# Kernel optimization log

Hardware: AMD Instinct MI355X
Metric: run time of the kernel (lower is better)

The kernel has to match this reference:

```python
import jax, jax.numpy as jnp
import numpy as np

# HGIN_classifier: two relational-GIN layers with ReLU between.
# FastRGIN layer math (relational GIN, eps=0, single-linear MLP):
#   agg_r[i] = sum_{(j->i) with edge_type r} x[j]          (per-relation neighbor sum)
#   out[i]   = (1+eps) * x[i] @ W_self + sum_r agg_r[i] @ W_r + b

N = 100000      # nodes
E = 1600000     # edges (avg degree 16)
R = 2           # relations (follower / following)
DIN, DH, DOUT = 128, 256, 2
EPS = 0.0


def setup_inputs() -> dict:
    key = jax.random.key(0)
    ks = jax.random.split(key, 8)
    x = jax.random.normal(ks[0], (N, DIN), dtype=jnp.float32)
    edge_index = jax.random.randint(ks[1], (2, E), 0, N, dtype=jnp.int64)
    edge_type = jax.random.randint(ks[2], (E,), 0, R, dtype=jnp.int64)
    s1 = 1.0 / np.sqrt(DIN).astype(np.float32)
    s2 = 1.0 / np.sqrt(DH).astype(np.float32)
    w1_self = jax.random.normal(ks[3], (DIN, DH), jnp.float32) * s1
    w1_rel = jax.random.normal(ks[4], (R, DIN, DH), jnp.float32) * s1
    b1 = jnp.zeros((DH,), jnp.float32)
    w2_self = jax.random.normal(ks[5], (DH, DOUT), jnp.float32) * s2
    w2_rel = jax.random.normal(ks[6], (R, DH, DOUT), jnp.float32) * s2
    b2 = jnp.zeros((DOUT,), jnp.float32)
    return {"x": x, "edge_index": edge_index, "edge_type": edge_type,
            "w1_self": w1_self, "w1_rel": w1_rel, "b1": b1,
            "w2_self": w2_self, "w2_rel": w2_rel, "b2": b2}


def _rgin_layer(x, src, dst, etype, w_self, w_rel, b):
    n = x.shape[0]
    r = w_rel.shape[0]
    # fused (node, relation) segment id so one segment_sum handles all relations
    seg = dst * r + etype                                   # [E]
    agg = jax.ops.segment_sum(x[src], seg, num_segments=n * r)  # [N*R, d_in]
    agg = agg.reshape(n, r, -1)                              # [N, R, d_in]
    return (1.0 + EPS) * (x @ w_self) + jnp.einsum('nri,rio->no', agg, w_rel) + b


def reference(x, edge_index, edge_type, w1_self, w1_rel, b1, w2_self, w2_rel, b2):
    src, dst = edge_index[0], edge_index[1]
    h = jax.nn.relu(_rgin_layer(x, src, dst, edge_type, w1_self, w1_rel, b1))
    out = _rgin_layer(h, src, dst, edge_type, w2_self, w2_rel, b2)
    return out
```

## Files before the change

kernel.cpp:

```cpp
#include <hip/hip_runtime.h>


typedef _Float16 f16;
typedef _Float16 f16x2 __attribute__((ext_vector_type(2)));
typedef _Float16 f16x4 __attribute__((ext_vector_type(4)));
typedef _Float16 f16x8 __attribute__((ext_vector_type(8)));
typedef float    f32x4 __attribute__((ext_vector_type(4)));

constexpr int NN   = 100000;
constexpr int NR   = NN * 2;
constexpr int NB   = 512;
constexpr int BSH  = 9;
constexpr int CHUNK = 8192;

__global__ void zero_small(int* __restrict__ gcnt) {
  int t = threadIdx.x;
  if (t < NB) gcnt[t] = 0;
}

__global__ void bucketA(const int* __restrict__ dst, const int* __restrict__ et,
                        int* __restrict__ gcnt, int E) {
  __shared__ int h[NB];
  int t = threadIdx.x;
  for (int b = t; b < NB; b += 256) h[b] = 0;
  __syncthreads();
  int lo = blockIdx.x * CHUNK, hi = min(E, lo + CHUNK);
  for (int e = lo + t; e < hi; e += 256)
    atomicAdd(&h[(dst[e] * 2 + et[e]) >> BSH], 1);
  __syncthreads();
  for (int b = t; b < NB; b += 256) {
    int c = h[b];
    if (c) atomicAdd(&gcnt[b], c);
  }
}

__global__ void bscan(const int* __restrict__ gcnt, int* __restrict__ bstart,
                      int* __restrict__ gbase) {
  __shared__ int s[NB];
  int t = threadIdx.x;
  int v = gcnt[t];
  s[t] = v;
  __syncthreads();
  #pragma unroll
  for (int o = 1; o < NB; o <<= 1) {
    int u = (t >= o) ? s[t - o] : 0;
    __syncthreads();
    s[t] += u;
    __syncthreads();
  }
  bstart[t] = s[t] - v;
  gbase[t]  = s[t] - v;
  if (t == NB - 1) bstart[NB] = s[t];
}

__global__ void bucketB(const int* __restrict__ src, const int* __restrict__ dst,
                        const int* __restrict__ et, int* __restrict__ gbase,
                        int2* __restrict__ ebuf, int E) {
  __shared__ int h[NB], base[NB];
  int t = threadIdx.x;
  for (int b = t; b < NB; b += 256) h[b] = 0;
  __syncthreads();
  int lo = blockIdx.x * CHUNK, hi = min(E, lo + CHUNK);
  for (int e = lo + t; e < hi; e += 256)
    atomicAdd(&h[(dst[e] * 2 + et[e]) >> BSH], 1);
  __syncthreads();
  for (int b = t; b < NB; b += 256) {
    int c = h[b];
    base[b] = c ? atomicAdd(&gbase[b], c) : 0;
    h[b] = 0;
  }
  __syncthreads();
  for (int e = lo + t; e < hi; e += 256) {
    int seg = dst[e] * 2 + et[e];
    int b = seg >> BSH;
    int r = atomicAdd(&h[b], 1);
    ebuf[base[b] + r] = make_int2(src[e], seg);
  }
}

__global__ void bucketC(const int2* __restrict__ ebuf, const int* __restrict__ bstart,
                        int* __restrict__ off, int* __restrict__ srcs) {
  __shared__ int sh[NB], soff[NB], cnt[NB], tmp[256];
  int b = blockIdx.x, t = threadIdx.x;
  int lo = bstart[b], hi = bstart[b + 1];
  for (int s0 = t; s0 < NB; s0 += 256) { sh[s0] = 0; cnt[s0] = 0; }
  __syncthreads();
  for (int e = lo + t; e < hi; e += 256)
    atomicAdd(&sh[ebuf[e].y - (b << BSH)], 1);
  __syncthreads();
  int a0 = sh[2 * t], a1 = sh[2 * t + 1];
  tmp[t] = a0 + a1;
  __syncthreads();
  #pragma unroll
  for (int o = 1; o < 256; o <<= 1) {
    int u = (t >= o) ? tmp[t - o] : 0;
    __syncthreads();
    tmp[t] += u;
    __syncthreads();
  }
  int ex = tmp[t] - (a0 + a1);
  soff[2 * t] = ex;
  soff[2 * t + 1] = ex + a0;
  __syncthreads();
  int g0 = (b << BSH) + 2 * t;
  if (g0 <= NR)     off[g0]     = lo + soff[2 * t];
  if (g0 + 1 <= NR) off[g0 + 1] = lo + soff[2 * t + 1];
  for (int e = lo + t; e < hi; e += 256) {
    int2 p = ebuf[e];
    int s = p.y - (b << BSH);
    int r = atomicAdd(&cnt[s], 1);
    srcs[lo + soff[s] + r] = p.x;
  }
}

__global__ void cvt_x(const float4* __restrict__ xf, f16* __restrict__ xh, int n4) {
  int i = blockIdx.x * blockDim.x + threadIdx.x;
  if (i >= n4) return;
  float4 v = xf[i];
  f16x4 h;
  h.x = (f16)v.x; h.y = (f16)v.y; h.z = (f16)v.z; h.w = (f16)v.w;
  *(f16x4*)(xh + (size_t)i * 4) = h;
}

__global__ void cvt_w(const float* __restrict__ w1s, const float* __restrict__ w1r,
                      f16* __restrict__ w1t) {
  int id = blockIdx.x * blockDim.x + threadIdx.x;
  if (id >= 12 * 256 * 32) return;
  int ks = id >> 13, rem = id & 8191;
  int n = rem >> 5, ki = rem & 31;
  int k = ks * 32 + ki;
  float v = (k < 128) ? w1s[k * 256 + n] : w1r[(k - 128) * 256 + n];
  w1t[id] = (f16)v;
}

__global__ void aggregate(const f16* __restrict__ xh, const int* __restrict__ off,
                          const int* __restrict__ srcs, f16* __restrict__ aggh) {
  int w = (blockIdx.x * blockDim.x + threadIdx.x) >> 6;
  if (w >= NN) return;
  int lane = threadIdx.x & 63;
  int e0 = off[2 * w];
  int e1 = off[2 * w + 1];
  int e2 = off[2 * w + 2];
  float a0 = 0.f, a1 = 0.f, c0 = 0.f, c1 = 0.f;
  int e = e0;
  for (; e + 3 < e1; e += 4) {
    f16x2 v0 = *(const f16x2*)(xh + (long)srcs[e] * 128 + lane * 2);
    f16x2 v1 = *(const f16x2*)(xh + (long)srcs[e + 1] * 128 + lane * 2);
    f16x2 v2 = *(const f16x2*)(xh + (long)srcs[e + 2] * 128 + lane * 2);
    f16x2 v3 = *(const f16x2*)(xh + (long)srcs[e + 3] * 128 + lane * 2);
    a0 += (float)v0.x + (float)v1.x + (float)v2.x + (float)v3.x;
    a1 += (float)v0.y + (float)v1.y + (float)v2.y + (float)v3.y;
  }
  for (; e < e1; ++e) {
    f16x2 v = *(const f16x2*)(xh + (long)srcs[e] * 128 + lane * 2);
    a0 += (float)v.x; a1 += (float)v.y;
  }
  e = e1;
  for (; e + 3 < e2; e += 4) {
    f16x2 v0 = *(const f16x2*)(xh + (long)srcs[e] * 128 + lane * 2);
    f16x2 v1 = *(const f16x2*)(xh + (long)srcs[e + 1] * 128 + lane * 2);
    f16x2 v2 = *(const f16x2*)(xh + (long)srcs[e + 2] * 128 + lane * 2);
    f16x2 v3 = *(const f16x2*)(xh + (long)srcs[e + 3] * 128 + lane * 2);
    c0 += (float)v0.x + (float)v1.x + (float)v2.x + (float)v3.x;
    c1 += (float)v0.y + (float)v1.y + (float)v2.y + (float)v3.y;
  }
  for (; e < e2; ++e) {
    f16x2 v = *(const f16x2*)(xh + (long)srcs[e] * 128 + lane * 2);
    c0 += (float)v.x; c1 += (float)v.y;
  }
  f16* row = aggh + (long)w * 256;
  f16x2 o0; o0.x = (f16)a0; o0.y = (f16)a1;
  f16x2 o1; o1.x = (f16)c0; o1.y = (f16)c1;
  *(f16x2*)(row + lane * 2) = o0;
  *(f16x2*)(row + 128 + lane * 2) = o1;
}

__global__ __launch_bounds__(256) void gemm_mfma(
    const f16* __restrict__ xh, const f16* __restrict__ aggh,
    const f16* __restrict__ w1t,
    const float* __restrict__ b1, const float* __restrict__ w2s,
    const float* __restrict__ w2r, const float* __restrict__ b2,
    float* __restrict__ z2, float* __restrict__ out) {
  __shared__ float zbuf[4][64][6];
  const int t = threadIdx.x;
  const int lane = t & 63, wv = t >> 6;
  const int ml = lane & 15, quad = lane >> 4;
  const long rowBase = (long)blockIdx.x * 64;

  long rowc[4];
  #pragma unroll
  for (int mt = 0; mt < 4; ++mt) {
    long r = rowBase + mt * 16 + ml;
    rowc[mt] = r < NN ? r : (NN - 1);
  }
  const f16* bbase = w1t + (long)(wv * 64 + ml) * 32 + quad * 8;

  f32x4 acc[4][4];
  #pragma unroll
  for (int mt = 0; mt < 4; ++mt)
    #pragma unroll
    for (int nt = 0; nt < 4; ++nt) acc[mt][nt] = (f32x4)(0.f);

  #pragma unroll
  for (int ks = 0; ks < 12; ++ks) {
    f16x8 af[4], bf[4];
    #pragma unroll
    for (int mt = 0; mt < 4; ++mt) {
      const f16* ap = (ks < 4)
          ? (xh + rowc[mt] * 128 + ks * 32 + quad * 8)
          : (aggh + rowc[mt] * 256 + (ks - 4) * 32 + quad * 8);
      af[mt] = *(const f16x8*)ap;
    }
    #pragma unroll
    for (int nt = 0; nt < 4; ++nt)
      bf[nt] = *(const f16x8*)(bbase + (long)ks * 8192 + nt * 16 * 32);
    #pragma unroll
    for (int mt = 0; mt < 4; ++mt)
      #pragma unroll
      for (int nt = 0; nt < 4; ++nt)
        acc[mt][nt] = __builtin_amdgcn_mfma_f32_16x16x32_f16(af[mt], bf[nt],
                                                             acc[mt][nt], 0, 0, 0);
  }

  #pragma unroll
  for (int mt = 0; mt < 4; ++mt) {
    float z[4][6];
    #pragma unroll
    for (int rr = 0; rr < 4; ++rr)
      #pragma unroll
      for (int p = 0; p < 6; ++p) z[rr][p] = 0.f;
    #pragma unroll
    for (int nt = 0; nt < 4; ++nt) {
      int col = wv * 64 + nt * 16 + ml;
      float bb = b1[col];
      float wA = w2r[col * 2 + 0];
      float wB = w2r[col * 2 + 1];
      float wC = w2r[512 + col * 2 + 0];
      float wD = w2r[512 + col * 2 + 1];
      float wE = w2s[col * 2 + 0];
      float wF = w2s[col * 2 + 1];
      #pragma unroll
      for (int rr = 0; rr < 4; ++rr) {
        float h = acc[mt][nt][rr] + bb;
        h = h > 0.f ? h : 0.f;
        z[rr][0] = fmaf(h, wA, z[rr][0]);
        z[rr][1] = fmaf(h, wB, z[rr][1]);
        z[rr][2] = fmaf(h, wC, z[rr][2]);
        z[rr][3] = fmaf(h, wD, z[rr][3]);
        z[rr][4] = fmaf(h, wE, z[rr][4]);
        z[rr][5] = fmaf(h, wF, z[rr][5]);
      }
    }
    #pragma unroll
    for (int rr = 0; rr < 4; ++rr)
      #pragma unroll
      for (int p = 0; p < 6; ++p) {
        float v = z[rr][p];
        v += __shfl_xor(v, 1);
        v += __shfl_xor(v, 2);
        v += __shfl_xor(v, 4);
        v += __shfl_xor(v, 8);
        if (ml == 0) zbuf[wv][mt * 16 + quad * 4 + rr][p] = v;
      }
  }
  __syncthreads();
  for (int i = t; i < 384; i += 256) {
    int r = i / 6, p = i % 6;
    long grow = rowBase + r;
    if (grow < NN) {
      float v = zbuf[0][r][p] + zbuf[1][r][p] + zbuf[2][r][p] + zbuf[3][r][p];
      if (p < 4) z2[grow * 4 + p] = v;
      else       out[grow * 2 + (p - 4)] = v + b2[p - 4];
    }
  }
}

__global__ void gather2(const float* __restrict__ z2, const int* __restrict__ off,
                        const int* __restrict__ srcs, float* __restrict__ out) {
  int tid = blockIdx.x * blockDim.x + threadIdx.x;
  int n = tid >> 2;
  if (n >= NN) return;
  int sub = tid & 3;
  int e0 = off[2 * n];
  int e1 = off[2 * n + 1];
  int e2 = off[2 * n + 2];
  float o0 = 0.f, o1 = 0.f;
  for (int e = e0 + sub; e < e1; e += 4) {
    float2 v = *(const float2*)(z2 + (long)srcs[e] * 4);
    o0 += v.x; o1 += v.y;
  }
  for (int e = e1 + sub; e < e2; e += 4) {
    float2 v = *(const float2*)(z2 + (long)srcs[e] * 4 + 2);
    o0 += v.x; o1 += v.y;
  }
  o0 += __shfl_xor(o0, 1); o1 += __shfl_xor(o1, 1);
  o0 += __shfl_xor(o0, 2); o1 += __shfl_xor(o1, 2);
  if (sub == 0) {
    out[n * 2 + 0] += o0;
    out[n * 2 + 1] += o1;
  }
}

extern "C" void kernel_launch(void* const* d_in, const int* in_sizes, int n_in,
                              void* d_out, int out_size, void* d_ws, size_t ws_size,
                              hipStream_t stream) {
  const float* x   = (const float*)d_in[0];
  const int*   ei  = (const int*)d_in[1];
  const int*   et  = (const int*)d_in[2];
  const float* w1s = (const float*)d_in[3];
  const float* w1r = (const float*)d_in[4];
  const float* b1  = (const float*)d_in[5];
  const float* w2s = (const float*)d_in[6];
  const float* w2r = (const float*)d_in[7];
  const float* b2  = (const float*)d_in[8];
  float* out = (float*)d_out;
  const int E = in_sizes[2];
  const int* src = ei;
  const int* dst = ei + E;

  f16*   aggh = (f16*)d_ws;
  f16*   xh   = aggh + (size_t)NN * 256;
  f16*   w1t  = xh + (size_t)NN * 128;
  float* z2   = (float*)(w1t + 12 * 256 * 32);
  int2*  ebuf = (int2*)(z2 + (size_t)NN * 4);
  int*   srcs = (int*)(ebuf + E);
  int*   off  = srcs + E;
  int*   gcnt = off + NR + 1;
  int*   bstart = gcnt + NB;
  int*   gbase  = bstart + NB + 1;

  int nblk = (E + CHUNK - 1) / CHUNK;
  zero_small<<<1, 512, 0, stream>>>(gcnt);
  bucketA<<<nblk, 256, 0, stream>>>(dst, et, gcnt, E);
  bscan<<<1, 512, 0, stream>>>(gcnt, bstart, gbase);
  bucketB<<<nblk, 256, 0, stream>>>(src, dst, et, gbase, ebuf, E);
  bucketC<<<NB, 256, 0, stream>>>(ebuf, bstart, off, srcs);

  int n4 = NN * 128 / 4;
  cvt_x<<<(n4 + 255) / 256, 256, 0, stream>>>((const float4*)x, xh, n4);
  cvt_w<<<(12 * 256 * 32 + 255) / 256, 256, 0, stream>>>(w1s, w1r, w1t);

  aggregate<<<(NN * 64 + 255) / 256, 256, 0, stream>>>(xh, off, srcs, aggh);

  gemm_mfma<<<(NN + 63) / 64, 256, 0, stream>>>(xh, aggh, w1t, b1, w2s, w2r, b2,
                                                z2, out);

  gather2<<<(NN * 4 + 255) / 256, 256, 0, stream>>>(z2, off, srcs, out);
}
```

Before: 385.9 us.

## Pack bucket entries, merge convert kernels, widen gathers, stage GEMM tiles in LDS

Bucket entries are packed into one int (src shifted left plus the local segment), which halves the ebuf traffic. The two conversion kernels become one launch. The aggregate kernel now has each half-wave load 8-byte f16x4 chunks of different edges and combines the halves with a cross-lane shuffle, so each load instruction fetches two neighbor rows. The layer-1 GEMM stages A and B tiles in padded, double-buffered LDS with register prefetch, replacing the per-wave direct global fragment loads, at the cost of extra barriers and more shared memory per block.

```diff
diff --git a/kernel.cpp b/kernel.cpp
--- a/kernel.cpp
+++ b/kernel.cpp
@@ -12,6 +12,7 @@
 constexpr int NB   = 512;
 constexpr int BSH  = 9;
 constexpr int CHUNK = 8192;
+constexpr int RP   = 40;
 
 __global__ void zero_small(int* __restrict__ gcnt) {
   int t = threadIdx.x;
@@ -55,7 +56,7 @@
 
 __global__ void bucketB(const int* __restrict__ src, const int* __restrict__ dst,
                         const int* __restrict__ et, int* __restrict__ gbase,
-                        int2* __restrict__ ebuf, int E) {
+                        int* __restrict__ ebuf, int E) {
   __shared__ int h[NB], base[NB];
   int t = threadIdx.x;
   for (int b = t; b < NB; b += 256) h[b] = 0;
@@ -74,11 +75,11 @@
     int seg = dst[e] * 2 + et[e];
     int b = seg >> BSH;
     int r = atomicAdd(&h[b], 1);
-    ebuf[base[b] + r] = make_int2(src[e], seg);
-  }
-}
-
-__global__ void bucketC(const int2* __restrict__ ebuf, const int* __restrict__ bstart,
+    ebuf[base[b] + r] = (src[e] << BSH) | (seg & (NB - 1));
+  }
+}
+
+__global__ void bucketC(const int* __restrict__ ebuf, const int* __restrict__ bstart,
                         int* __restrict__ off, int* __restrict__ srcs) {
   __shared__ int sh[NB], soff[NB], cnt[NB], tmp[256];
   int b = blockIdx.x, t = threadIdx.x;
@@ -86,7 +87,7 @@
   for (int s0 = t; s0 < NB; s0 += 256) { sh[s0] = 0; cnt[s0] = 0; }
   __syncthreads();
   for (int e = lo + t; e < hi; e += 256)
-    atomicAdd(&sh[ebuf[e].y - (b << BSH)], 1);
+    atomicAdd(&sh[ebuf[e] & (NB - 1)], 1);
   __syncthreads();
   int a0 = sh[2 * t], a1 = sh[2 * t + 1];
   tmp[t] = a0 + a1;
@@ -106,31 +107,32 @@
   if (g0 <= NR)     off[g0]     = lo + soff[2 * t];
   if (g0 + 1 <= NR) off[g0 + 1] = lo + soff[2 * t + 1];
   for (int e = lo + t; e < hi; e += 256) {
-    int2 p = ebuf[e];
-    int s = p.y - (b << BSH);
+    int p = ebuf[e];
+    int s = p & (NB - 1);
     int r = atomicAdd(&cnt[s], 1);
-    srcs[lo + soff[s] + r] = p.x;
-  }
-}
-
-__global__ void cvt_x(const float4* __restrict__ xf, f16* __restrict__ xh, int n4) {
+    srcs[lo + soff[s] + r] = ((unsigned)p) >> BSH;
+  }
+}
+
+__global__ void cvt_all(const float4* __restrict__ xf, f16* __restrict__ xh,
+                        const float* __restrict__ w1s, const float* __restrict__ w1r,
+                        f16* __restrict__ w1t, int n4) {
   int i = blockIdx.x * blockDim.x + threadIdx.x;
-  if (i >= n4) return;
-  float4 v = xf[i];
-  f16x4 h;
-  h.x = (f16)v.x; h.y = (f16)v.y; h.z = (f16)v.z; h.w = (f16)v.w;
-  *(f16x4*)(xh + (size_t)i * 4) = h;
-}
-
-__global__ void cvt_w(const float* __restrict__ w1s, const float* __restrict__ w1r,
-                      f16* __restrict__ w1t) {
-  int id = blockIdx.x * blockDim.x + threadIdx.x;
-  if (id >= 12 * 256 * 32) return;
-  int ks = id >> 13, rem = id & 8191;
-  int n = rem >> 5, ki = rem & 31;
-  int k = ks * 32 + ki;
-  float v = (k < 128) ? w1s[k * 256 + n] : w1r[(k - 128) * 256 + n];
-  w1t[id] = (f16)v;
+  if (i < n4) {
+    float4 v = xf[i];
+    f16x4 h;
+    h.x = (f16)v.x; h.y = (f16)v.y; h.z = (f16)v.z; h.w = (f16)v.w;
+    *(f16x4*)(xh + (size_t)i * 4) = h;
+  } else {
+    int id = i - n4;
+    if (id < 12 * 256 * 32) {
+      int ks = id >> 13, rem = id & 8191;
+      int n = rem >> 5, ki = rem & 31;
+      int k = ks * 32 + ki;
+      float v = (k < 128) ? w1s[k * 256 + n] : w1r[(k - 128) * 256 + n];
+      w1t[id] = (f16)v;
+    }
+  }
 }
 
 __global__ void aggregate(const f16* __restrict__ xh, const int* __restrict__ off,
@@ -138,41 +140,66 @@
   int w = (blockIdx.x * blockDim.x + threadIdx.x) >> 6;
   if (w >= NN) return;
   int lane = threadIdx.x & 63;
+  int h = lane >> 5, c = lane & 31;
   int e0 = off[2 * w];
   int e1 = off[2 * w + 1];
   int e2 = off[2 * w + 2];
-  float a0 = 0.f, a1 = 0.f, c0 = 0.f, c1 = 0.f;
+  float ax = 0.f, ay = 0.f, az = 0.f, aw = 0.f;
+  float bx = 0.f, by = 0.f, bz = 0.f, bw = 0.f;
+
   int e = e0;
-  for (; e + 3 < e1; e += 4) {
-    f16x2 v0 = *(const f16x2*)(xh + (long)srcs[e] * 128 + lane * 2);
-    f16x2 v1 = *(const f16x2*)(xh + (long)srcs[e + 1] * 128 + lane * 2);
-    f16x2 v2 = *(const f16x2*)(xh + (long)srcs[e + 2] * 128 + lane * 2);
-    f16x2 v3 = *(const f16x2*)(xh + (long)srcs[e + 3] * 128 + lane * 2);
-    a0 += (float)v0.x + (float)v1.x + (float)v2.x + (float)v3.x;
-    a1 += (float)v0.y + (float)v1.y + (float)v2.y + (float)v3.y;
-  }
-  for (; e < e1; ++e) {
-    f16x2 v = *(const f16x2*)(xh + (long)srcs[e] * 128 + lane * 2);
-    a0 += (float)v.x; a1 += (float)v.y;
+  for (; e + 7 < e1; e += 8) {
+    f16x4 v0 = *(const f16x4*)(xh + (long)srcs[e     + h] * 128 + c * 4);
+    f16x4 v1 = *(const f16x4*)(xh + (long)srcs[e + 2 + h] * 128 + c * 4);
+    f16x4 v2 = *(const f16x4*)(xh + (long)srcs[e + 4 + h] * 128 + c * 4);
+    f16x4 v3 = *(const f16x4*)(xh + (long)srcs[e + 6 + h] * 128 + c * 4);
+    ax += (float)v0.x + (float)v1.x + (float)v2.x + (float)v3.x;
+    ay += (float)v0.y + (float)v1.y + (float)v2.y + (float)v3.y;
+    az += (float)v0.z + (float)v1.z + (float)v2.z + (float)v3.z;
+    aw += (float)v0.w + (float)v1.w + (float)v2.w + (float)v3.w;
+  }
+  for (; e + 1 < e1; e += 2) {
+    f16x4 v = *(const f16x4*)(xh + (long)srcs[e + h] * 128 + c * 4);
+    ax += (float)v.x; ay += (float)v.y; az += (float)v.z; aw += (float)v.w;
+  }
+  if (e < e1) {
+    f16x4 v = *(const f16x4*)(xh + (long)srcs[e] * 128 + c * 4);
+    if (h == 0) { ax += (float)v.x; ay += (float)v.y; az += (float)v.z; aw += (float)v.w; }
   }
   e = e1;
-  for (; e + 3 < e2; e += 4) {
-    f16x2 v0 = *(const f16x2*)(xh + (long)srcs[e] * 128 + lane * 2);
-    f16x2 v1 = *(const f16x2*)(xh + (long)srcs[e + 1] * 128 + lane * 2);
-    f16x2 v2 = *(const f16x2*)(xh + (long)srcs[e + 2] * 128 + lane * 2);
-    f16x2 v3 = *(const f16x2*)(xh + (long)srcs[e + 3] * 128 + lane * 2);
-    c0 += (float)v0.x + (float)v1.x + (float)v2.x + (float)v3.x;
-    c1 += (float)v0.y + (float)v1.y + (float)v2.y + (float)v3.y;
-  }
-  for (; e < e2; ++e) {
-    f16x2 v = *(const f16x2*)(xh + (long)srcs[e] * 128 + lane * 2);
-    c0 += (float)v.x; c1 += (float)v.y;
-  }
+  for (; e + 7 < e2; e += 8) {
+    f16x4 v0 = *(const f16x4*)(xh + (long)srcs[e     + h] * 128 + c * 4);
+    f16x4 v1 = *(const f16x4*)(xh + (long)srcs[e + 2 + h] * 128 + c * 4);
+    f16x4 v2 = *(const f16x4*)(xh + (long)srcs[e + 4 + h] * 128 + c * 4);
+    f16x4 v3 = *(const f16x4*)(xh + (long)srcs[e + 6 + h] * 128 + c * 4);
+    bx += (float)v0.x + (float)v1.x + (float)v2.x + (float)v3.x;
+    by += (float)v0.y + (float)v1.y + (float)v2.y + (float)v3.y;
+    bz += (float)v0.z + (float)v1.z + (float)v2.z + (float)v3.z;
+    bw += (float)v0.w + (float)v1.w + (float)v2.w + (float)v3.w;
+  }
+  for (; e + 1 < e2; e += 2) {
+    f16x4 v = *(const f16x4*)(xh + (long)srcs[e + h] * 128 + c * 4);
+    bx += (float)v.x; by += (float)v.y; bz += (float)v.z; bw += (float)v.w;
+  }
+  if (e < e2) {
+    f16x4 v = *(const f16x4*)(xh + (long)srcs[e] * 128 + c * 4);
+    if (h == 0) { bx += (float)v.x; by += (float)v.y; bz += (float)v.z; bw += (float)v.w; }
+  }
+
+  ax += __shfl_xor(ax, 32); ay += __shfl_xor(ay, 32);
+  az += __shfl_xor(az, 32); aw += __shfl_xor(aw, 32);
+  bx += __shfl_xor(bx, 32); by += __shfl_xor(by, 32);
+  bz += __shfl_xor(bz, 32); bw += __shfl_xor(bw, 32);
+
   f16* row = aggh + (long)w * 256;
-  f16x2 o0; o0.x = (f16)a0; o0.y = (f16)a1;
-  f16x2 o1; o1.x = (f16)c0; o1.y = (f16)c1;
-  *(f16x2*)(row + lane * 2) = o0;
-  *(f16x2*)(row + 128 + lane * 2) = o1;
+  f16x4 o;
+  if (h == 0) {
+    o.x = (f16)ax; o.y = (f16)ay; o.z = (f16)az; o.w = (f16)aw;
+    *(f16x4*)(row + c * 4) = o;
+  } else {
+    o.x = (f16)bx; o.y = (f16)by; o.z = (f16)bz; o.w = (f16)bw;
+    *(f16x4*)(row + 128 + c * 4) = o;
+  }
 }
 
 __global__ __launch_bounds__(256) void gemm_mfma(
@@ -181,19 +208,15 @@
     const float* __restrict__ b1, const float* __restrict__ w2s,
     const float* __restrict__ w2r, const float* __restrict__ b2,
     float* __restrict__ z2, float* __restrict__ out) {
-  __shared__ float zbuf[4][64][6];
+  __shared__ __align__(16) f16 Ash[2][64 * RP];
+  __shared__ __align__(16) f16 Bsh[2][256 * RP];
+  float (*zbuf)[64][6] = (float (*)[64][6])(void*)Bsh;
   const int t = threadIdx.x;
   const int lane = t & 63, wv = t >> 6;
   const int ml = lane & 15, quad = lane >> 4;
   const long rowBase = (long)blockIdx.x * 64;
-
-  long rowc[4];
-  #pragma unroll
-  for (int mt = 0; mt < 4; ++mt) {
-    long r = rowBase + mt * 16 + ml;
-    rowc[mt] = r < NN ? r : (NN - 1);
-  }
-  const f16* bbase = w1t + (long)(wv * 64 + ml) * 32 + quad * 8;
+  const int ar = t >> 2, ach = t & 3;
+  const long agrow = (rowBase + ar < NN) ? rowBase + ar : (NN - 1);
 
   f32x4 acc[4][4];
   #pragma unroll
@@ -201,26 +224,50 @@
     #pragma unroll
     for (int nt = 0; nt < 4; ++nt) acc[mt][nt] = (f32x4)(0.f);
 
-  #pragma unroll
+  uint4 av, bv[4];
+  auto load_tile = [&](int ks) {
+    const f16* ap = (ks < 4)
+        ? (xh + agrow * 128 + ks * 32 + ach * 8)
+        : (aggh + agrow * 256 + (ks - 4) * 32 + ach * 8);
+    av = *(const uint4*)ap;
+    const uint4* bp = (const uint4*)(w1t + (long)ks * 8192) + t * 4;
+    #pragma unroll
+    for (int c = 0; c < 4; ++c) bv[c] = bp[c];
+  };
+  auto store_tile = [&](int buf) {
+    *(uint4*)&Ash[buf][ar * RP + ach * 8] = av;
+    #pragma unroll
+    for (int c = 0; c < 4; ++c) *(uint4*)&Bsh[buf][t * RP + c * 8] = bv[c];
+  };
+
+  load_tile(0);
+  store_tile(0);
+  __syncthreads();
+
   for (int ks = 0; ks < 12; ++ks) {
+    const int cur = ks & 1;
+    if (ks < 11) load_tile(ks + 1);
+
     f16x8 af[4], bf[4];
     #pragma unroll
-    for (int mt = 0; mt < 4; ++mt) {
-      const f16* ap = (ks < 4)
-          ? (xh + rowc[mt] * 128 + ks * 32 + quad * 8)
-          : (aggh + rowc[mt] * 256 + (ks - 4) * 32 + quad * 8);
-      af[mt] = *(const f16x8*)ap;
-    }
+    for (int mt = 0; mt < 4; ++mt)
+      af[mt] = *(const f16x8*)&Ash[cur][(mt * 16 + ml) * RP + quad * 8];
     #pragma unroll
     for (int nt = 0; nt < 4; ++nt)
-      bf[nt] = *(const f16x8*)(bbase + (long)ks * 8192 + nt * 16 * 32);
+      bf[nt] = *(const f16x8*)&Bsh[cur][(wv * 64 + nt * 16 + ml) * RP + quad * 8];
     #pragma unroll
     for (int mt = 0; mt < 4; ++mt)
       #pragma unroll
       for (int nt = 0; nt < 4; ++nt)
         acc[mt][nt] = __builtin_amdgcn_mfma_f32_16x16x32_f16(af[mt], bf[nt],
                                                              acc[mt][nt], 0, 0, 0);
-  }
+    if (ks < 11) {
+      __syncthreads();
+      store_tile(1 - cur);
+      __syncthreads();
+    }
+  }
+  __syncthreads();
 
   #pragma unroll
   for (int mt = 0; mt < 4; ++mt) {
@@ -241,14 +288,14 @@
       float wF = w2s[col * 2 + 1];
       #pragma unroll
       for (int rr = 0; rr < 4; ++rr) {
-        float h = acc[mt][nt][rr] + bb;
-        h = h > 0.f ? h : 0.f;
-        z[rr][0] = fmaf(h, wA, z[rr][0]);
-        z[rr][1] = fmaf(h, wB, z[rr][1]);
-        z[rr][2] = fmaf(h, wC, z[rr][2]);
-        z[rr][3] = fmaf(h, wD, z[rr][3]);
-        z[rr][4] = fmaf(h, wE, z[rr][4]);
-        z[rr][5] = fmaf(h, wF, z[rr][5]);
+        float hh = acc[mt][nt][rr] + bb;
+        hh = hh > 0.f ? hh : 0.f;
+        z[rr][0] = fmaf(hh, wA, z[rr][0]);
+        z[rr][1] = fmaf(hh, wB, z[rr][1]);
+        z[rr][2] = fmaf(hh, wC, z[rr][2]);
+        z[rr][3] = fmaf(hh, wD, z[rr][3]);
+        z[rr][4] = fmaf(hh, wE, z[rr][4]);
+        z[rr][5] = fmaf(hh, wF, z[rr][5]);
       }
     }
     #pragma unroll
@@ -322,8 +369,8 @@
   f16*   xh   = aggh + (size_t)NN * 256;
   f16*   w1t  = xh + (size_t)NN * 128;
   float* z2   = (float*)(w1t + 12 * 256 * 32);
-  int2*  ebuf = (int2*)(z2 + (size_t)NN * 4);
-  int*   srcs = (int*)(ebuf + E);
+  int*   ebuf = (int*)(z2 + (size_t)NN * 4);
+  int*   srcs = ebuf + E;
   int*   off  = srcs + E;
   int*   gcnt = off + NR + 1;
   int*   bstart = gcnt + NB;
@@ -337,8 +384,9 @@
   bucketC<<<NB, 256, 0, stream>>>(ebuf, bstart, off, srcs);
 
   int n4 = NN * 128 / 4;
-  cvt_x<<<(n4 + 255) / 256, 256, 0, stream>>>((const float4*)x, xh, n4);
-  cvt_w<<<(12 * 256 * 32 + 255) / 256, 256, 0, stream>>>(w1s, w1r, w1t);
+  int ncvt = n4 + 12 * 256 * 32;
+  cvt_all<<<(ncvt + 255) / 256, 256, 0, stream>>>((const float4*)x, xh,
+                                                  w1s, w1r, w1t, n4);
 
   aggregate<<<(NN * 64 + 255) / 256, 256, 0, stream>>>(xh, off, srcs, aggh);
 
```

Measured after the change: 415.7 us. +7.7%, slower.
